# Performance work log

Hardware: AMD Instinct MI355X
Metric: run time of the kernel (lower is better)

The kernel has to match this reference:

```python
import math
import jax, jax.numpy as jnp
import numpy as np

N_HEADS = 16
NUM_BUCKETS = 32
MAX_DISTANCE = 128


def _relative_position_bucket(relative_positions, num_buckets=NUM_BUCKETS, max_distance=MAX_DISTANCE):
    # bidirectional=True branch of the torch helper
    ret = -relative_positions
    nb = num_buckets // 2
    sign = (ret < 0).astype(jnp.int32)
    ret = jnp.abs(ret)
    max_exact = nb // 2
    is_small = ret < max_exact
    # torch .long() truncates toward zero; values in the selected (large) branch are >= 0 so int cast matches
    large = max_exact + jnp.minimum(
        (jnp.log(ret.astype(jnp.float32) / max_exact + 1e-6)
         / math.log(max_distance / max_exact) * (nb - max_exact)).astype(jnp.int32),
        nb - max_exact - 1,
    )
    return jnp.where(is_small, ret, large) + sign * nb


def setup_inputs() -> dict:
    key = jax.random.key(0)
    k1, k2, k3, k4, k5 = jax.random.split(key, 5)
    d_model = 1024
    B, L = 2, 2048
    return {
        "query": jax.random.normal(k1, (B, L, d_model), dtype=jnp.float32),
        "Wq": jax.random.normal(k2, (d_model, d_model), dtype=jnp.float32) * 0.02,
        "Wkv": jax.random.normal(k3, (d_model, 2 * d_model), dtype=jnp.float32) * 0.02,
        "Wo": jax.random.normal(k4, (d_model, d_model), dtype=jnp.float32) * 0.02,
        "rel_bias": jax.random.normal(k5, (N_HEADS * NUM_BUCKETS, 1), dtype=jnp.float32) * 0.02,
    }


def reference(query, Wq, Wkv, Wo, rel_bias):
    B, L, D = query.shape
    H = N_HEADS
    hd = D // H
    scale = 1.0 / math.sqrt(hd)

    q = query @ Wq                      # [B, L, D]
    kv = query @ Wkv                    # [B, L, 2D]
    k, v = jnp.split(kv, 2, axis=-1)

    def split_heads(x):
        return x.reshape(B, L, H, hd).transpose(0, 2, 1, 3)  # [B, H, L, hd]

    q, k, v = map(split_heads, (q, k, v))

    scores = jnp.einsum("bhqd,bhkd->bhqk", q, k) * scale      # [B, H, L, L]

    # relative position bias
    pos = jnp.arange(L)
    rp = pos[None, :] - pos[:, None]                           # mem - ctx, [L, L]
    buckets = _relative_position_bucket(rp)                    # [L, L]
    idx = buckets[None, :, :] + (jnp.arange(H) * NUM_BUCKETS)[:, None, None]  # [H, L, L]
    bias = rel_bias[idx, 0][None]                              # [1, H, L, L]

    attn = jax.nn.softmax(scores + bias, axis=-1)
    out = jnp.einsum("bhqk,bhkd->bhqd", attn, v)               # [B, H, L, hd]
    out = out.transpose(0, 2, 1, 3).reshape(B, L, D) @ Wo      # [B, L, D]
    return out, bias
```

## Files before the change

### kernel.cpp

```cpp
#include <hip/hip_runtime.h>


typedef unsigned short u16;
typedef unsigned int u32;
typedef __attribute__((ext_vector_type(4))) float f32x4;
typedef __attribute__((ext_vector_type(8))) short bf16x8;
typedef __attribute__((ext_vector_type(4))) unsigned short u16x4;

#define MFMA16(a, b, c) __builtin_amdgcn_mfma_f32_16x16x32_bf16(a, b, c, 0, 0, 0)

typedef const __attribute__((address_space(1))) void gvoid;
typedef __attribute__((address_space(3))) void lvoid;
static __device__ __forceinline__ void gll16(const void* g, void* l) {
    __builtin_amdgcn_global_load_lds((gvoid*)g, (lvoid*)l, 16, 0, 0);
}

static __device__ inline u16 f2bf(float f) {
    u32 x = __float_as_uint(f);
    x += 0x7fffu + ((x >> 16) & 1u);
    return (u16)(x >> 16);
}
static __device__ inline u32 pk2(float a, float b) {
    return (u32)f2bf(a) | ((u32)f2bf(b) << 16);
}

__global__ __launch_bounds__(256) void prep(
    const float* __restrict__ X, const float* __restrict__ Wq,
    const float* __restrict__ Wkv, const float* __restrict__ Wo,
    const float* __restrict__ rel_bias, u16* __restrict__ Xb,
    u16* __restrict__ Wt, float* __restrict__ tbl)
{
    __shared__ u16 T[64 * 72];
    const int bx = blockIdx.x, tid = threadIdx.x;
    if (bx < 2048) {
        int i = (bx * 256 + tid) * 8;
        float4 a = *(const float4*)(X + i);
        float4 b = *(const float4*)(X + i + 4);
        uint4 w = { pk2(a.x, a.y), pk2(a.z, a.w), pk2(b.x, b.y), pk2(b.z, b.w) };
        *(uint4*)(Xb + i) = w;
    } else if (bx < 3072) {
        int bx2 = bx - 2048;
        int k0 = (bx2 & 15) * 64;
        int n0 = (bx2 >> 4) * 64;
        const float* src; int ld, nb;
        if (n0 < 1024)      { src = Wq;  ld = 1024; nb = n0; }
        else if (n0 < 3072) { src = Wkv; ld = 2048; nb = n0 - 1024; }
        else                { src = Wo;  ld = 1024; nb = n0 - 3072; }
        const int r0 = tid >> 4, c4 = (tid & 15) * 4;
        for (int rr = 0; rr < 4; rr++) {
            int row = rr * 16 + r0;
            float4 f = *(const float4*)(src + (size_t)(k0 + row) * ld + nb + c4);
            T[(c4 + 0) * 72 + row] = f2bf(f.x);
            T[(c4 + 1) * 72 + row] = f2bf(f.y);
            T[(c4 + 2) * 72 + row] = f2bf(f.z);
            T[(c4 + 3) * 72 + row] = f2bf(f.w);
        }
        __syncthreads();
        const int n = tid >> 2, ks0 = (tid & 3) * 16;
        uint4 u0 = *(const uint4*)&T[n * 72 + ks0];
        uint4 u1 = *(const uint4*)&T[n * 72 + ks0 + 8];
        uint4* d = (uint4*)(Wt + (size_t)(n0 + n) * 1024 + k0 + ks0);
        d[0] = u0; d[1] = u1;
    } else {
        int i = (bx - 3072) * 256 + tid;
        int rel = (i & 4095) - 2047;
        int h = i >> 12;
        int ret = -rel;
        int sign = (ret < 0) ? 1 : 0;
        int aret = (ret < 0) ? -ret : ret;
        int bucket;
        if (aret < 8) {
            bucket = aret;
        } else {
            float v = (logf((float)aret * 0.125f + 1e-6f) / logf(16.0f)) * 8.0f;
            int iv = (int)v;
            bucket = 8 + (iv < 7 ? iv : 7);
        }
        bucket += sign * 16;
        tbl[i] = rel_bias[h * 32 + bucket];
    }
}

__global__ __launch_bounds__(256) void qkv_gemm(
    const u16* __restrict__ Xb, const u16* __restrict__ Wt,
    u16* __restrict__ qws, u16* __restrict__ kws, u16* __restrict__ vtws)
{
    __shared__ u16 As[128 * 64];
    __shared__ u16 Bs[128 * 64];
    const int tid = threadIdx.x;
    const int n0 = blockIdx.x * 128;
    const int m0 = blockIdx.y * 128;
    const int wid = tid >> 6, lane = tid & 63, c = lane & 15, quad = lane >> 4;
    const int wm = (wid >> 1) * 64, wn = (wid & 1) * 64;
    const f32x4 z = {0.f, 0.f, 0.f, 0.f};
    f32x4 acc[4][4];
    for (int i = 0; i < 4; i++) for (int j = 0; j < 4; j++) acc[i][j] = z;
    const int rsub = lane >> 3;
    const int dchunk = (lane & 7) ^ (rsub & 7);
    const u16* ag = Xb + (size_t)(m0 + wid * 32 + rsub) * 1024 + dchunk * 8;
    const u16* bg = Wt + (size_t)(n0 + wid * 32 + rsub) * 1024 + dchunk * 8;
    u16* lA = &As[(wid * 32) * 64];
    u16* lB = &Bs[(wid * 32) * 64];
    const int sw = c & 7;

    for (int kk = 0; kk < 1024; kk += 64) {
        for (int i = 0; i < 4; i++)
            gll16(ag + (size_t)i * 8 * 1024 + kk, lA + i * 8 * 64);
        for (int i = 0; i < 4; i++)
            gll16(bg + (size_t)i * 8 * 1024 + kk, lB + i * 8 * 64);
        __syncthreads();
        for (int ks = 0; ks < 2; ks++) {
            const int sl = ((ks * 4 + quad) ^ sw) * 8;
            bf16x8 af[4], bfr[4];
            for (int im = 0; im < 4; im++)
                af[im] = *(const bf16x8*)&As[(wm + im * 16 + c) * 64 + sl];
            for (int jn = 0; jn < 4; jn++)
                bfr[jn] = *(const bf16x8*)&Bs[(wn + jn * 16 + c) * 64 + sl];
            for (int im = 0; im < 4; im++)
                for (int jn = 0; jn < 4; jn++)
                    acc[im][jn] = MFMA16(af[im], bfr[jn], acc[im][jn]);
        }
        __syncthreads();
    }
    for (int im = 0; im < 4; im++) for (int jn = 0; jn < 4; jn++) {
        int gm0 = m0 + wm + im * 16 + quad * 4;
        int gn = n0 + wn + jn * 16 + c;
        if (gn < 2048) {
            u16* dstbase = (gn < 1024) ? qws : kws;
            int nn = gn & 1023;
            int h = nn >> 6, d = nn & 63;
            for (int r = 0; r < 4; r++) {
                int gm = gm0 + r, bb = gm >> 11, l = gm & 2047;
                dstbase[(((size_t)bb * 16 + h) * 2048 + l) * 64 + d] = f2bf(acc[im][jn][r]);
            }
        } else {
            int nn = gn - 2048;
            int h = nn >> 6, d = nn & 63;
            int bb = gm0 >> 11, l = gm0 & 2047;
            u16x4 pk = { f2bf(acc[im][jn][0]), f2bf(acc[im][jn][1]),
                         f2bf(acc[im][jn][2]), f2bf(acc[im][jn][3]) };
            *(u16x4*)&vtws[(((size_t)bb * 16 + h) * 64 + d) * 2048 + l] = pk;
        }
    }
}

__global__ __launch_bounds__(256, 2) void attn_kernel(
    const u16* __restrict__ qws, const u16* __restrict__ kws,
    const u16* __restrict__ vtws, const float* __restrict__ tbl,
    u16* __restrict__ ows, float* __restrict__ bias_out)
{
    __shared__ u16 QPs[128 * 72];
    __shared__ u16 Ks[2][64 * 64];
    __shared__ u16 Vt[2][64 * 64];
    __shared__ float Bw[2][192];
    const int tid = threadIdx.x;
    const int qt = blockIdx.x, bh = blockIdx.y;
    const int b = bh >> 4, h = bh & 15;
    const u16* qp = qws + (size_t)bh * 2048 * 64;
    const u16* kp = kws + (size_t)bh * 2048 * 64;
    const u16* vp = vtws + (size_t)bh * 64 * 2048;
    const float* tb = tbl + h * 4096;
    const int q0 = qt * 128;
    const int wid = tid >> 6, lane = tid & 63, c = lane & 15, quad = lane >> 4;
    const int qw0 = wid * 32;
    const int sw = c & 7;
    const int rsub = lane >> 3;
    const int schunk = (lane & 7) ^ rsub;
    const int birow = tid >> 3, bjj = (tid & 7) * 4;

    auto stage = [&](int buf, int k0) {
        for (int g = 0; g < 2; g++) {
            gll16(kp + (size_t)(k0 + wid * 16 + g * 8 + rsub) * 64 + schunk * 8,
                  &Ks[buf][(wid * 16 + g * 8) * 64]);
            gll16(vp + (size_t)(wid * 16 + g * 8 + rsub) * 2048 + k0 + schunk * 8,
                  &Vt[buf][(wid * 16 + g * 8) * 64]);
        }
        if (tid < 192) Bw[buf][tid] = tb[k0 - q0 + 1920 + tid] * 1.44269504f;
    };

    stage(0, 0);
    {
        int row = tid >> 1, c0 = (tid & 1) * 32;
        const uint4* s = (const uint4*)(qp + (size_t)(q0 + row) * 64 + c0);
        uint4 v0 = s[0], v1 = s[1], v2 = s[2], v3 = s[3];
        uint4* d = (uint4*)&QPs[row * 72 + c0];
        d[0] = v0; d[1] = v1; d[2] = v2; d[3] = v3;
    }
    __syncthreads();
    bf16x8 bq[2][2];
    for (int nt = 0; nt < 2; nt++)
        for (int ks = 0; ks < 2; ks++)
            bq[nt][ks] = *(const bf16x8*)&QPs[(qw0 + nt * 16 + c) * 72 + ks * 32 + quad * 8];
    __syncthreads();
    u16* Ps = QPs + wid * (32 * 72);

    float lrow[2] = { 0.f, 0.f };
    const f32x4 z = {0.f, 0.f, 0.f, 0.f};
    f32x4 accO[2][4];
    for (int i = 0; i < 2; i++) for (int j = 0; j < 4; j++) accO[i][j] = z;

    for (int kt = 0; kt < 32; kt++) {
        const int cur = kt & 1;
        const int k0 = kt * 64;
        if (kt < 31) stage(cur ^ 1, k0 + 64);
        f32x4 accS[4][2];
        for (int i = 0; i < 4; i++) { accS[i][0] = z; accS[i][1] = z; }
        for (int ks = 0; ks < 2; ks++)
            for (int ktile = 0; ktile < 4; ktile++) {
                bf16x8 ak = *(const bf16x8*)
                    &Ks[cur][(ktile * 16 + c) * 64 + (((ks * 4 + quad) ^ sw)) * 8];
                accS[ktile][0] = MFMA16(ak, bq[0][ks], accS[ktile][0]);
                accS[ktile][1] = MFMA16(ak, bq[1][ks], accS[ktile][1]);
            }
        float rsum[2] = { 0.f, 0.f };
        for (int ktile = 0; ktile < 4; ktile++)
            for (int nt = 0; nt < 2; nt++) {
                const float* bp = &Bw[cur][ktile * 16 + quad * 4 - qw0 - nt * 16 - c + 127];
                float p0 = exp2f(fmaf(accS[ktile][nt][0], 0.180336878f, bp[0]));
                float p1 = exp2f(fmaf(accS[ktile][nt][1], 0.180336878f, bp[1]));
                float p2 = exp2f(fmaf(accS[ktile][nt][2], 0.180336878f, bp[2]));
                float p3 = exp2f(fmaf(accS[ktile][nt][3], 0.180336878f, bp[3]));
                rsum[nt] += (p0 + p1) + (p2 + p3);
                u16x4 pk = { f2bf(p0), f2bf(p1), f2bf(p2), f2bf(p3) };
                *(u16x4*)&Ps[(nt * 16 + c) * 72 + ktile * 16 + quad * 4] = pk;
            }
        lrow[0] += rsum[0]; lrow[1] += rsum[1];
        for (int kb = 0; kb < 2; kb++) {
            bf16x8 bv[4];
            for (int nt = 0; nt < 4; nt++)
                bv[nt] = *(const bf16x8*)
                    &Vt[cur][(nt * 16 + c) * 64 + (((kb * 4 + quad) ^ sw)) * 8];
            for (int mt = 0; mt < 2; mt++) {
                bf16x8 ap = *(const bf16x8*)&Ps[(mt * 16 + c) * 72 + kb * 32 + quad * 8];
                for (int nt = 0; nt < 4; nt++)
                    accO[mt][nt] = MFMA16(ap, bv[nt], accO[mt][nt]);
            }
        }
        {
            const int jbase = k0 + b * 32 + bjj;
            const float* tw = tb + (jbase + 2047 - q0);
            float* dstb = bias_out + ((size_t)h * 2048 + q0 + birow) * 2048 + jbase;
            for (int rr = 0; rr < 4; rr++) {
                const float* twp = tw - (birow + rr * 32);
                f32x4 v = { twp[0], twp[1], twp[2], twp[3] };
                __builtin_nontemporal_store(v, (f32x4*)(dstb + (size_t)rr * 32 * 2048));
            }
        }
        __syncthreads();
    }
    for (int nt = 0; nt < 2; nt++) {
        lrow[nt] += __shfl_xor(lrow[nt], 16, 64);
        lrow[nt] += __shfl_xor(lrow[nt], 32, 64);
    }
    for (int mt = 0; mt < 2; mt++)
        for (int r = 0; r < 4; r++) {
            float lq = __shfl(lrow[mt], quad * 4 + r, 64);
            float rl = 1.0f / lq;
            int qg = q0 + qw0 + mt * 16 + quad * 4 + r;
            size_t base = ((size_t)b * 2048 + qg) * 1024 + h * 64;
            for (int nt = 0; nt < 4; nt++)
                ows[base + nt * 16 + c] = f2bf(accO[mt][nt][r] * rl);
        }
}

__global__ __launch_bounds__(256) void out_gemm(
    const u16* __restrict__ O, const u16* __restrict__ Wot, float* __restrict__ out)
{
    __shared__ u16 As[128 * 64];
    __shared__ u16 Bs[128 * 64];
    const int tid = threadIdx.x;
    const int n0 = blockIdx.x * 128;
    const int m0 = blockIdx.y * 128;
    const int wid = tid >> 6, lane = tid & 63, c = lane & 15, quad = lane >> 4;
    const int wm = (wid >> 1) * 64, wn = (wid & 1) * 64;
    const f32x4 z = {0.f, 0.f, 0.f, 0.f};
    f32x4 acc[4][4];
    for (int i = 0; i < 4; i++) for (int j = 0; j < 4; j++) acc[i][j] = z;
    const int rsub = lane >> 3;
    const int dchunk = (lane & 7) ^ (rsub & 7);
    const u16* ag = O + (size_t)(m0 + wid * 32 + rsub) * 1024 + dchunk * 8;
    const u16* bg = Wot + (size_t)(n0 + wid * 32 + rsub) * 1024 + dchunk * 8;
    u16* lA = &As[(wid * 32) * 64];
    u16* lB = &Bs[(wid * 32) * 64];
    const int sw = c & 7;
    for (int kk = 0; kk < 1024; kk += 64) {
        for (int i = 0; i < 4; i++)
            gll16(ag + (size_t)i * 8 * 1024 + kk, lA + i * 8 * 64);
        for (int i = 0; i < 4; i++)
            gll16(bg + (size_t)i * 8 * 1024 + kk, lB + i * 8 * 64);
        __syncthreads();
        for (int ks = 0; ks < 2; ks++) {
            const int sl = ((ks * 4 + quad) ^ sw) * 8;
            bf16x8 af[4], bfr[4];
            for (int im = 0; im < 4; im++)
                af[im] = *(const bf16x8*)&As[(wm + im * 16 + c) * 64 + sl];
            for (int jn = 0; jn < 4; jn++)
                bfr[jn] = *(const bf16x8*)&Bs[(wn + jn * 16 + c) * 64 + sl];
            for (int im = 0; im < 4; im++)
                for (int jn = 0; jn < 4; jn++)
                    acc[im][jn] = MFMA16(af[im], bfr[jn], acc[im][jn]);
        }
        __syncthreads();
    }
    for (int im = 0; im < 4; im++) for (int jn = 0; jn < 4; jn++) {
        int gm0 = m0 + wm + im * 16 + quad * 4;
        int gn = n0 + wn + jn * 16 + c;
        for (int r = 0; r < 4; r++)
            __builtin_nontemporal_store(acc[im][jn][r], &out[(size_t)(gm0 + r) * 1024 + gn]);
    }
}

extern "C" void kernel_launch(void* const* d_in, const int* in_sizes, int n_in,
                              void* d_out, int out_size, void* d_ws, size_t ws_size,
                              hipStream_t stream)
{
    (void)in_sizes; (void)n_in; (void)out_size; (void)ws_size;
    const float* query    = (const float*)d_in[0];
    const float* Wq       = (const float*)d_in[1];
    const float* Wkv      = (const float*)d_in[2];
    const float* Wo       = (const float*)d_in[3];
    const float* rel_bias = (const float*)d_in[4];
    float* out = (float*)d_out;

    float* tbl = (float*)d_ws;
    u16* Xb   = (u16*)((char*)d_ws + 262144);
    u16* Wt   = Xb + 4194304;
    u16* qws  = Wt + 4194304;
    u16* kws  = qws + 4194304;
    u16* vtws = kws + 4194304;
    u16* ows  = vtws + 4194304;

    prep<<<3328, 256, 0, stream>>>(query, Wq, Wkv, Wo, rel_bias, Xb, Wt, tbl);
    qkv_gemm<<<dim3(24, 32), 256, 0, stream>>>(Xb, Wt, qws, kws, vtws);
    attn_kernel<<<dim3(16, 32), 256, 0, stream>>>(qws, kws, vtws, tbl, ows,
                                                  out + 4194304);
    out_gemm<<<dim3(8, 32), 256, 0, stream>>>(ows, Wt + (size_t)3072 * 1024, out);
}
```

Baseline: 405.6 us.

## Double-buffer LDS tiles in QKV and output projection GEMMs

Both projection GEMMs now hold two LDS buffers for the A and B tiles and issue the global-to-LDS loads for the next k-step before running MFMAs on the current one, with a single barrier per iteration. The aim is to hide global load latency behind matrix math. In exchange, shared memory per block doubles and launch bounds request two blocks per CU, which can cut occupancy and add register pressure. GEMMs are a smaller part of the total next to attention.

```diff
diff --git a/kernel.cpp b/kernel.cpp
--- a/kernel.cpp
+++ b/kernel.cpp
@@ -81,12 +81,12 @@
     }
 }
 
-__global__ __launch_bounds__(256) void qkv_gemm(
+__global__ __launch_bounds__(256, 2) void qkv_gemm(
     const u16* __restrict__ Xb, const u16* __restrict__ Wt,
     u16* __restrict__ qws, u16* __restrict__ kws, u16* __restrict__ vtws)
 {
-    __shared__ u16 As[128 * 64];
-    __shared__ u16 Bs[128 * 64];
+    __shared__ u16 As[2][128 * 64];
+    __shared__ u16 Bs[2][128 * 64];
     const int tid = threadIdx.x;
     const int n0 = blockIdx.x * 128;
     const int m0 = blockIdx.y * 128;
@@ -96,26 +96,30 @@
     f32x4 acc[4][4];
     for (int i = 0; i < 4; i++) for (int j = 0; j < 4; j++) acc[i][j] = z;
     const int rsub = lane >> 3;
-    const int dchunk = (lane & 7) ^ (rsub & 7);
+    const int dchunk = (lane & 7) ^ rsub;
     const u16* ag = Xb + (size_t)(m0 + wid * 32 + rsub) * 1024 + dchunk * 8;
     const u16* bg = Wt + (size_t)(n0 + wid * 32 + rsub) * 1024 + dchunk * 8;
-    u16* lA = &As[(wid * 32) * 64];
-    u16* lB = &Bs[(wid * 32) * 64];
     const int sw = c & 7;
 
-    for (int kk = 0; kk < 1024; kk += 64) {
+    auto stage = [&](int buf, int kk) {
         for (int i = 0; i < 4; i++)
-            gll16(ag + (size_t)i * 8 * 1024 + kk, lA + i * 8 * 64);
+            gll16(ag + (size_t)i * 8 * 1024 + kk, &As[buf][(wid * 32 + i * 8) * 64]);
         for (int i = 0; i < 4; i++)
-            gll16(bg + (size_t)i * 8 * 1024 + kk, lB + i * 8 * 64);
-        __syncthreads();
+            gll16(bg + (size_t)i * 8 * 1024 + kk, &Bs[buf][(wid * 32 + i * 8) * 64]);
+    };
+
+    stage(0, 0);
+    __syncthreads();
+    for (int it = 0; it < 16; it++) {
+        const int cur = it & 1;
+        if (it < 15) stage(cur ^ 1, (it + 1) * 64);
         for (int ks = 0; ks < 2; ks++) {
             const int sl = ((ks * 4 + quad) ^ sw) * 8;
             bf16x8 af[4], bfr[4];
             for (int im = 0; im < 4; im++)
-                af[im] = *(const bf16x8*)&As[(wm + im * 16 + c) * 64 + sl];
+                af[im] = *(const bf16x8*)&As[cur][(wm + im * 16 + c) * 64 + sl];
             for (int jn = 0; jn < 4; jn++)
-                bfr[jn] = *(const bf16x8*)&Bs[(wn + jn * 16 + c) * 64 + sl];
+                bfr[jn] = *(const bf16x8*)&Bs[cur][(wn + jn * 16 + c) * 64 + sl];
             for (int im = 0; im < 4; im++)
                 for (int jn = 0; jn < 4; jn++)
                     acc[im][jn] = MFMA16(af[im], bfr[jn], acc[im][jn]);
@@ -263,11 +267,11 @@
         }
 }
 
-__global__ __launch_bounds__(256) void out_gemm(
+__global__ __launch_bounds__(256, 2) void out_gemm(
     const u16* __restrict__ O, const u16* __restrict__ Wot, float* __restrict__ out)
 {
-    __shared__ u16 As[128 * 64];
-    __shared__ u16 Bs[128 * 64];
+    __shared__ u16 As[2][128 * 64];
+    __shared__ u16 Bs[2][128 * 64];
     const int tid = threadIdx.x;
     const int n0 = blockIdx.x * 128;
     const int m0 = blockIdx.y * 128;
@@ -277,25 +281,30 @@
     f32x4 acc[4][4];
     for (int i = 0; i < 4; i++) for (int j = 0; j < 4; j++) acc[i][j] = z;
     const int rsub = lane >> 3;
-    const int dchunk = (lane & 7) ^ (rsub & 7);
+    const int dchunk = (lane & 7) ^ rsub;
     const u16* ag = O + (size_t)(m0 + wid * 32 + rsub) * 1024 + dchunk * 8;
     const u16* bg = Wot + (size_t)(n0 + wid * 32 + rsub) * 1024 + dchunk * 8;
-    u16* lA = &As[(wid * 32) * 64];
-    u16* lB = &Bs[(wid * 32) * 64];
     const int sw = c & 7;
-    for (int kk = 0; kk < 1024; kk += 64) {
+
+    auto stage = [&](int buf, int kk) {
         for (int i = 0; i < 4; i++)
-            gll16(ag + (size_t)i * 8 * 1024 + kk, lA + i * 8 * 64);
+            gll16(ag + (size_t)i * 8 * 1024 + kk, &As[buf][(wid * 32 + i * 8) * 64]);
         for (int i = 0; i < 4; i++)
-            gll16(bg + (size_t)i * 8 * 1024 + kk, lB + i * 8 * 64);
-        __syncthreads();
+            gll16(bg + (size_t)i * 8 * 1024 + kk, &Bs[buf][(wid * 32 + i * 8) * 64]);
+    };
+
+    stage(0, 0);
+    __syncthreads();
+    for (int it = 0; it < 16; it++) {
+        const int cur = it & 1;
+        if (it < 15) stage(cur ^ 1, (it + 1) * 64);
         for (int ks = 0; ks < 2; ks++) {
             const int sl = ((ks * 4 + quad) ^ sw) * 8;
             bf16x8 af[4], bfr[4];
             for (int im = 0; im < 4; im++)
-                af[im] = *(const bf16x8*)&As[(wm + im * 16 + c) * 64 + sl];
+                af[im] = *(const bf16x8*)&As[cur][(wm + im * 16 + c) * 64 + sl];
             for (int jn = 0; jn < 4; jn++)
-                bfr[jn] = *(const bf16x8*)&Bs[(wn + jn * 16 + c) * 64 + sl];
+                bfr[jn] = *(const bf16x8*)&Bs[cur][(wn + jn * 16 + c) * 64 + sl];
             for (int im = 0; im < 4; im++)
                 for (int jn = 0; jn < 4; jn++)
                     acc[im][jn] = MFMA16(af[im], bfr[jn], acc[im][jn]);
```

New measurement: 419.2 us. +3.4%, slower.
